# Optimization experiments

Measured on AMD Instinct MI355X. Metric: run time of the kernel, lower is better.

The kernel has to match this reference:

```python
import jax, jax.numpy as jnp
import numpy as np

N_HEADS = 2
WINDOW = 4
BLOCK = 256


def _get_rel_emb(emb, length):
    # emb: [1, 2*WINDOW+1, K] -> [1, 2*length-1, K]
    pad = max(length - (WINDOW + 1), 0)
    start = max((WINDOW + 1) - length, 0)
    e = jnp.pad(emb, ((0, 0), (pad, pad), (0, 0)))
    return e[:, start:start + 2 * length - 1]


def _rel_to_abs(x):
    # x: [b, h, l, 2l-1] -> [b, h, l, l] (skew trick)
    b, h, l, _ = x.shape
    x = jnp.pad(x, ((0, 0), (0, 0), (0, 0), (0, 1))).reshape(b, h, 2 * l * l)
    x = jnp.pad(x, ((0, 0), (0, 0), (0, l - 1))).reshape(b, h, l + 1, 2 * l - 1)
    return x[:, :, :l, l - 1:]


def _abs_to_rel(x):
    # x: [b, h, l, l] -> [b, h, l, 2l-1] (inverse skew)
    b, h, l, _ = x.shape
    x = jnp.pad(x, ((0, 0), (0, 0), (0, 0), (0, l - 1))).reshape(b, h, l * (2 * l - 1))
    x = jnp.pad(x, ((0, 0), (0, 0), (l, 0))).reshape(b, h, l, 2 * l)
    return x[:, :, :, 1:]


def _attention(x, c, attn_mask, Wq, bq, Wk, bk, Wv, bv, Wo, bo, emb_rel_k, emb_rel_v):
    B, C, T = x.shape
    H, K = N_HEADS, C // N_HEADS
    # projections (torch Linear on [B,T,C])
    q = (jnp.einsum('bct,cd->btd', x, Wq) + bq).reshape(B, T, H, K).transpose(0, 2, 1, 3)
    k = (jnp.einsum('bct,cd->btd', c, Wk) + bk).reshape(B, T, H, K).transpose(0, 2, 1, 3)
    v = (jnp.einsum('bct,cd->btd', c, Wv) + bv).reshape(B, T, H, K).transpose(0, 2, 1, 3)
    qs = q / jnp.sqrt(jnp.float32(K))
    scores = jnp.einsum('bhtk,bhsk->bhts', qs, k)  # [B,H,T,T]
    # relative-position key logits (heads_share=True -> single table)
    rel_k = _get_rel_emb(emb_rel_k, T)[0]          # [2T-1, K]
    rel_logits = jnp.einsum('bhtk,rk->bhtr', qs, rel_k)
    scores = scores + _rel_to_abs(rel_logits)
    # proximal bias: -log1p(|i-j|)
    r = jnp.arange(T, dtype=jnp.float32)
    scores = scores - jnp.log1p(jnp.abs(r[:, None] - r[None, :]))[None, None]
    # attn mask + block-local mask (block mask active because mask is given)
    ij = jnp.arange(T)
    block_ok = jnp.abs(ij[:, None] - ij[None, :]) <= BLOCK
    valid = (attn_mask != 0) & block_ok[None, None]
    scores = jnp.where(valid, scores, jnp.float32(-1e4))
    p = jax.nn.softmax(scores, axis=-1)
    out = jnp.einsum('bhts,bhsk->bhtk', p, v)
    # relative-position value contribution
    rel_v = _get_rel_emb(emb_rel_v, T)[0]          # [2T-1, K]
    out = out + jnp.einsum('bhtr,rk->bhtk', _abs_to_rel(p), rel_v)
    out = out.transpose(0, 2, 1, 3).reshape(B, T, C)
    y = jnp.einsum('btd,do->bto', out, Wo) + bo
    return y.transpose(0, 2, 1)  # [B, out_channels, T]


def setup_inputs() -> dict:
    key = jax.random.key(0)
    ks = jax.random.split(key, 8)
    B, C, T = 4, 192, 2048
    K = C // N_HEADS
    s = jnp.float32(0.05)
    rel_std = jnp.float32(K ** -0.5)
    return {
        'x': jax.random.normal(ks[0], (B, C, T), jnp.float32),
        'c': jax.random.normal(ks[1], (B, C, T), jnp.float32),
        'Wq': jax.random.normal(ks[2], (C, C), jnp.float32) * s,
        'bq': jnp.zeros((C,), jnp.float32),
        'Wk': jax.random.normal(ks[3], (C, C), jnp.float32) * s,
        'bk': jnp.zeros((C,), jnp.float32),
        'Wv': jax.random.normal(ks[4], (C, C), jnp.float32) * s,
        'bv': jnp.zeros((C,), jnp.float32),
        'Wo': jax.random.normal(ks[5], (C, C), jnp.float32) * s,
        'bo': jnp.zeros((C,), jnp.float32),
        'emb_rel_k': jax.random.normal(ks[6], (1, 2 * WINDOW + 1, K), jnp.float32) * rel_std,
        'emb_rel_v': jax.random.normal(ks[7], (1, 2 * WINDOW + 1, K), jnp.float32) * rel_std,
        'attn_mask': jnp.ones((B, 1, T, T), jnp.int32),
    }


def reference(x, c, Wq, bq, Wk, bk, Wv, bv, Wo, bo, emb_rel_k, emb_rel_v, attn_mask):
    return _attention(x, c, attn_mask, Wq, bq, Wk, bk, Wv, bv, Wo, bo, emb_rel_k, emb_rel_v)
```

## Files before the change

kernel.cpp:

```cpp
#include <hip/hip_runtime.h>
#include <hip/hip_bf16.h>

#define B_DIM 4
#define C_DIM 192
#define T_SEQ 2048
#define H_DIM 2
#define K_DIM 96
#define BAND 256
#define IT 32
#define NJT 34
#define WSLOT 544
#define WPD 556
#define PRS (2*WPD)
#define XSTR 200
#define PDS 40

typedef __attribute__((ext_vector_type(8))) short bf16x8;
typedef __attribute__((ext_vector_type(4))) short bf16x4;
typedef __attribute__((ext_vector_type(4))) float f32x4;
#define MFMA16 __builtin_amdgcn_mfma_f32_16x16x32_bf16

__device__ __forceinline__ short f2bf_bits(float f) {
    union { __hip_bfloat16 h; short s; } u; u.h = __float2bfloat16(f); return u.s;
}

#define OFF_WT(m)  ((size_t)(m)*73728)
#define OFF_BQS    ((size_t)294912)
#define OFF_RELKBF ((size_t)295680)
#define OFF_RVT    ((size_t)298752)
#define OFF_QBF    ((size_t)304896)
#define OFF_KBF    (OFF_QBF + 3145728)
#define OFF_VTB    (OFF_KBF + 3145728)
#define OFF_OBTC   (OFF_VTB + 3145728)

__global__ __launch_bounds__(256)
void prep_kernel(const float* __restrict__ Wq, const float* __restrict__ Wk,
                 const float* __restrict__ Wv, const float* __restrict__ Wo,
                 const float* __restrict__ bq, const float* __restrict__ relk,
                 const float* __restrict__ relv, char* __restrict__ ws)
{
    const float qscale = 0.14724445972f;
    const int bidx = blockIdx.x;
    const int tid  = threadIdx.x;

    if (bidx < 144) {
        __shared__ float tile[32][33];
        const int mi = bidx / 36, tl = bidx % 36;
        const int R0 = (tl / 6) * 32, C0 = (tl % 6) * 32;
        const float* src = (mi == 0) ? Wq : (mi == 1) ? Wk : (mi == 2) ? Wv : Wo;
        const int r = tid >> 5, cc = tid & 31;
        #pragma unroll
        for (int i = 0; i < 4; ++i) {
            const int rr = r + 8*i;
            tile[rr][cc] = src[(R0 + rr)*C_DIM + C0 + cc];
        }
        __syncthreads();
        short* dst = (short*)(ws + OFF_WT(mi));
        #pragma unroll
        for (int i = 0; i < 4; ++i) {
            const int rr = r + 8*i;
            float v = tile[cc][rr];
            if (mi == 0) v *= qscale;
            dst[(C0 + rr)*C_DIM + R0 + cc] = f2bf_bits(v);
        }
        return;
    }
    if (tid < C_DIM)
        ((float*)(ws + OFF_BQS))[tid] = bq[tid]*qscale;
    short* rkb = (short*)(ws + OFF_RELKBF);
    for (int idx = tid; idx < 16*K_DIM; idx += 256) {
        const int row = idx / K_DIM;
        rkb[idx] = (row < 9) ? f2bf_bits(relk[idx]) : (short)0;
    }
    short* rvt = (short*)(ws + OFF_RVT);
    for (int idx = tid; idx < K_DIM*32; idx += 256) {
        const int col = idx >> 5, dd = idx & 31;
        rvt[idx] = (dd < 9) ? f2bf_bits(relv[dd*K_DIM + col]) : (short)0;
    }
}

__global__ __launch_bounds__(256)
void proj_kernel(const float* __restrict__ x, const float* __restrict__ cin,
                 const float* __restrict__ bk, const float* __restrict__ bv,
                 char* __restrict__ ws)
{
    __shared__ short sb[2*IT*XSTR/2];
    const int hw = blockIdx.x;
    const int L  = (hw & 7)*96 + (hw >> 3);
    const int which = L % 3;
    const int rest  = L / 3;
    const int b  = rest >> 6;
    const int t0 = (rest & 63) * 32;
    const int tid = threadIdx.x;
    const int wave = tid >> 6, lane = tid & 63;
    const int q4 = lane >> 4, lr = lane & 15;

    const float* src = (which == 0) ? x : cin;
    for (int l = tid; l < 1536; l += 256) {
        const int cr = l >> 3, u = l & 7;
        const float4 v4 = *reinterpret_cast<const float4*>(
            src + (size_t)(b*C_DIM + cr)*T_SEQ + t0 + 4*u);
        sb[(4*u+0)*XSTR + cr] = f2bf_bits(v4.x);
        sb[(4*u+1)*XSTR + cr] = f2bf_bits(v4.y);
        sb[(4*u+2)*XSTR + cr] = f2bf_bits(v4.z);
        sb[(4*u+3)*XSTR + cr] = f2bf_bits(v4.w);
    }
    __syncthreads();

    const short* WT = (const short*)(ws + OFF_WT(which));
    f32x4 a[3][2];
    #pragma unroll
    for (int j = 0; j < 3; ++j) {
        a[j][0] = (f32x4){0.f,0.f,0.f,0.f};
        a[j][1] = (f32x4){0.f,0.f,0.f,0.f};
    }
    for (int kc = 0; kc < 6; ++kc) {
        const int ko = kc*32 + q4*8;
        const bf16x8 sf0 = *reinterpret_cast<const bf16x8*>(sb + lr*XSTR + ko);
        const bf16x8 sf1 = *reinterpret_cast<const bf16x8*>(sb + (16 + lr)*XSTR + ko);
        #pragma unroll
        for (int j = 0; j < 3; ++j) {
            const bf16x8 wf = *reinterpret_cast<const bf16x8*>(
                WT + ((3*wave + j)*16 + lr)*C_DIM + ko);
            if (which == 2) {
                a[j][0] = MFMA16(wf, sf0, a[j][0], 0, 0, 0);
                a[j][1] = MFMA16(wf, sf1, a[j][1], 0, 0, 0);
            } else {
                a[j][0] = MFMA16(sf0, wf, a[j][0], 0, 0, 0);
                a[j][1] = MFMA16(sf1, wf, a[j][1], 0, 0, 0);
            }
        }
    }

    const float* bqs = (const float*)(ws + OFF_BQS);
    #pragma unroll
    for (int j = 0; j < 3; ++j) {
        const int dt = 3*wave + j;
        if (which <= 1) {
            const int d = dt*16 + lr, h = d/K_DIM, kk = d%K_DIM;
            const int bh = b*H_DIM + h;
            const float bias = (which == 0) ? bqs[d] : bk[d];
            short* dst = (short*)(ws + (which == 0 ? OFF_QBF : OFF_KBF));
            #pragma unroll
            for (int rt = 0; rt < 2; ++rt)
                #pragma unroll
                for (int e = 0; e < 4; ++e) {
                    const int t = t0 + rt*16 + q4*4 + e;
                    dst[((size_t)bh*T_SEQ + t)*K_DIM + kk] = f2bf_bits(a[j][rt][e] + bias);
                }
        } else {
            short* vtb = (short*)(ws + OFF_VTB);
            #pragma unroll
            for (int rt = 0; rt < 2; ++rt)
                #pragma unroll
                for (int e = 0; e < 4; ++e) {
                    const int d = dt*16 + q4*4 + e, h = d/K_DIM, kk = d%K_DIM;
                    const int bh = b*H_DIM + h;
                    vtb[((size_t)bh*K_DIM + kk)*T_SEQ + t0 + rt*16 + lr] =
                        f2bf_bits(a[j][rt][e] + bv[d]);
                }
        }
    }
}

__global__ __launch_bounds__(1024, 8)
void attn_kernel(const int* __restrict__ mask, char* __restrict__ ws)
{
    __shared__ __align__(16) float ps[IT*WPD];
    __shared__ float lt[257];
    __shared__ __align__(16) char upool[2560];
    float* rl   = (float*)upool;
    short* pd_s = (short*)upool;

    const short* qbf = (const short*)(ws + OFF_QBF);
    const short* kbf = (const short*)(ws + OFF_KBF);
    const short* vtb = (const short*)(ws + OFF_VTB);
    const short* rkb = (const short*)(ws + OFF_RELKBF);
    const short* rvt = (const short*)(ws + OFF_RVT);
    short* obtc = (short*)(ws + OFF_OBTC);

    const int L    = ((blockIdx.x & 7) << 6) + (blockIdx.x >> 3);
    const int b    = L >> 7;
    const int rem  = L & 127;
    const int i0   = (rem >> 1) * IT;
    const int head = rem & 1;
    const int tid  = threadIdx.x;
    const int wave = tid >> 6, lane = tid & 63;
    const int q4 = lane >> 4, lr = lane & 15;
    const int ri = wave & 1, wg = wave >> 1;

    const int jlo  = max(0, i0 - BAND);
    const int jhi  = min(T_SEQ - 1, i0 + IT - 1 + BAND);
    const int wlen = jhi - jlo + 1;
    const size_t qk_base = (size_t)(b*H_DIM + head) * T_SEQ * K_DIM;

    for (int idx = tid; idx < 257; idx += 1024) lt[idx] = log2f((float)(1 + idx));

    bf16x8 qa[3];
    {
        const short* qrow = qbf + qk_base + (size_t)(i0 + ri*16 + lr)*K_DIM + q4*8;
        #pragma unroll
        for (int kc = 0; kc < 3; ++kc)
            qa[kc] = *reinterpret_cast<const bf16x8*>(qrow + kc*32);
    }

    for (int jt = wg; jt < NJT; jt += 8) {
        int jr = jlo + jt*16 + lr;
        if (jr > T_SEQ-1) jr = T_SEQ-1;
        const short* krow = kbf + qk_base + (size_t)jr*K_DIM + q4*8;
        f32x4 s = {0.f,0.f,0.f,0.f};
        #pragma unroll
        for (int kc = 0; kc < 3; ++kc)
            s = MFMA16(qa[kc], *reinterpret_cast<const bf16x8*>(krow + kc*32), s, 0, 0, 0);
        float* pr = ps + (ri*16 + q4*4)*WPD + jt*16 + lr;
        pr[0*WPD] = s[0]; pr[1*WPD] = s[1]; pr[2*WPD] = s[2]; pr[3*WPD] = s[3];
    }
    if (wg == 7) {
        const short* krow = rkb + lr*K_DIM + q4*8;
        f32x4 rs = {0.f,0.f,0.f,0.f};
        #pragma unroll
        for (int kc = 0; kc < 3; ++kc)
            rs = MFMA16(qa[kc], *reinterpret_cast<const bf16x8*>(krow + kc*32), rs, 0, 0, 0);
        if (lr < 9) {
            #pragma unroll
            for (int e = 0; e < 4; ++e)
                rl[(ri*16 + q4*4 + e)*9 + lr] = rs[e];
        }
    }
    __syncthreads();

    {
        const int r = tid >> 5, sj = tid & 31;
        const int i = i0 + r;
        const int* mrow = mask + ((size_t)b*T_SEQ + i)*T_SEQ;
        float* prow = ps + r*WPD;
        float vals[20];
        float m = -INFINITY;
        #pragma unroll
        for (int mm = 0; mm < 5; ++mm) {
            const int j0 = 4*sj + 128*mm;
            float4 pv = make_float4(0.f,0.f,0.f,0.f);
            int4 mv = make_int4(0,0,0,0);
            if (j0 < wlen) {
                pv = *reinterpret_cast<const float4*>(prow + j0);
                mv = *reinterpret_cast<const int4*>(mrow + jlo + j0);
            }
            const float pe[4] = {pv.x, pv.y, pv.z, pv.w};
            const int me[4] = {mv.x, mv.y, mv.z, mv.w};
            #pragma unroll
            for (int e = 0; e < 4; ++e) {
                const int j = j0 + e;
                float val = -INFINITY;
                if (j0 < wlen && j < wlen) {
                    const int dd = jlo + j - i;
                    const int ad = dd < 0 ? -dd : dd;
                    if (ad <= BAND && me[e] != 0) {
                        val = pe[e] - lt[ad];
                        if ((unsigned)(dd + 4) <= 8u) val += rl[r*9 + dd + 4];
                    }
                }
                vals[mm*4 + e] = val;
                m = fmaxf(m, val);
            }
        }
        #pragma unroll
        for (int off = 16; off > 0; off >>= 1) m = fmaxf(m, __shfl_xor(m, off, 64));
        if (m == -INFINITY) m = 0.f;
        float ssum = 0.f;
        #pragma unroll
        for (int u = 0; u < 20; ++u) { vals[u] = exp2f(vals[u] - m); ssum += vals[u]; }
        #pragma unroll
        for (int off = 16; off > 0; off >>= 1) ssum += __shfl_xor(ssum, off, 64);
        const float inv = ssum > 0.f ? 1.f/ssum : 0.f;
        short* pbrow = (short*)prow;
        #pragma unroll
        for (int mm = 0; mm < 5; ++mm) {
            const int j0 = 4*sj + 128*mm;
            if (j0 < WSLOT) {
                bf16x4 w;
                #pragma unroll
                for (int e = 0; e < 4; ++e) w[e] = f2bf_bits(vals[mm*4+e]*inv);
                *reinterpret_cast<bf16x4*>(pbrow + j0) = w;
            }
        }
    }
    __syncthreads();

    for (int idx = tid; idx < IT*PDS; idx += 1024) {
        const int r = idx / PDS, kk = idx % PDS;
        short v = 0;
        if (kk < 9) {
            const int jg = i0 + r + kk - 4;
            if (jg >= 0 && jg < T_SEQ)
                v = ((const short*)ps)[r*PRS + (jg - jlo)];
        }
        pd_s[idx] = v;
    }

    f32x4 o = {0.f,0.f,0.f,0.f};
    const int pri = wave & 1, pnt = wave >> 1;
    if (wave < 12) {
        const short* pbh = (const short*)ps;
        const short* vbase = vtb + qk_base + (size_t)(pnt*16 + lr)*T_SEQ;
        for (int kc = 0; kc < NJT/2; ++kc) {
            const bf16x8 pa = *reinterpret_cast<const bf16x8*>(
                pbh + (pri*16 + lr)*PRS + kc*32 + q4*8);
            int tc = jlo + kc*32 + q4*8;
            if (tc > T_SEQ-8) tc = T_SEQ-8;
            const bf16x8 vb = *reinterpret_cast<const bf16x8*>(vbase + tc);
            o = MFMA16(pa, vb, o, 0, 0, 0);
        }
    }
    __syncthreads();

    if (wave < 12) {
        const bf16x8 pda = *reinterpret_cast<const bf16x8*>(pd_s + (pri*16 + lr)*PDS + q4*8);
        const bf16x8 rv  = *reinterpret_cast<const bf16x8*>(rvt + (pnt*16 + lr)*32 + q4*8);
        o = MFMA16(pda, rv, o, 0, 0, 0);
        const int col = head*K_DIM + pnt*16 + lr;
        #pragma unroll
        for (int e = 0; e < 4; ++e) {
            const int i = i0 + pri*16 + q4*4 + e;
            obtc[((size_t)b*T_SEQ + i)*C_DIM + col] = f2bf_bits(o[e]);
        }
    }
}

__global__ __launch_bounds__(256)
void oproj_kernel(const float* __restrict__ bo, float* __restrict__ y,
                  const char* __restrict__ ws)
{
    const int bid = ((blockIdx.x & 7) << 5) + (blockIdx.x >> 3);
    const int b   = bid >> 6;
    const int t0  = (bid & 63) * 32;
    const int tid = threadIdx.x;
    const int wave = tid >> 6, lane = tid & 63;
    const int q4 = lane >> 4, lr = lane & 15;

    const short* WoT  = (const short*)(ws + OFF_WT(3));
    const short* obtc = (const short*)(ws + OFF_OBTC);

    f32x4 a[3][2];
    #pragma unroll
    for (int j = 0; j < 3; ++j) {
        a[j][0] = (f32x4){0.f,0.f,0.f,0.f};
        a[j][1] = (f32x4){0.f,0.f,0.f,0.f};
    }
    for (int kc = 0; kc < 6; ++kc) {
        const int ko = kc*32 + q4*8;
        const bf16x8 bf0 = *reinterpret_cast<const bf16x8*>(
            obtc + ((size_t)b*T_SEQ + t0 + lr)*C_DIM + ko);
        const bf16x8 bf1 = *reinterpret_cast<const bf16x8*>(
            obtc + ((size_t)b*T_SEQ + t0 + 16 + lr)*C_DIM + ko);
        #pragma unroll
        for (int j = 0; j < 3; ++j) {
            const bf16x8 af = *reinterpret_cast<const bf16x8*>(
                WoT + ((3*wave + j)*16 + lr)*C_DIM + ko);
            a[j][0] = MFMA16(af, bf0, a[j][0], 0, 0, 0);
            a[j][1] = MFMA16(af, bf1, a[j][1], 0, 0, 0);
        }
    }
    #pragma unroll
    for (int j = 0; j < 3; ++j) {
        #pragma unroll
        for (int rt = 0; rt < 2; ++rt)
            #pragma unroll
            for (int e = 0; e < 4; ++e) {
                const int d = (3*wave + j)*16 + q4*4 + e;
                y[((size_t)b*C_DIM + d)*T_SEQ + t0 + rt*16 + lr] = a[j][rt][e] + bo[d];
            }
    }
}

extern "C" void kernel_launch(void* const* d_in, const int* in_sizes, int n_in,
                              void* d_out, int out_size, void* d_ws, size_t ws_size,
                              hipStream_t stream)
{
    const float* x    = (const float*)d_in[0];
    const float* c    = (const float*)d_in[1];
    const float* Wq   = (const float*)d_in[2];
    const float* bq   = (const float*)d_in[3];
    const float* Wk   = (const float*)d_in[4];
    const float* bk   = (const float*)d_in[5];
    const float* Wv   = (const float*)d_in[6];
    const float* bv   = (const float*)d_in[7];
    const float* Wo   = (const float*)d_in[8];
    const float* bo   = (const float*)d_in[9];
    const float* relk = (const float*)d_in[10];
    const float* relv = (const float*)d_in[11];
    const int*   mask = (const int*)d_in[12];
    float*       y    = (float*)d_out;
    char*        ws   = (char*)d_ws;

    hipLaunchKernelGGL(prep_kernel, dim3(145), dim3(256), 0, stream,
                       Wq, Wk, Wv, Wo, bq, relk, relv, ws);
    hipLaunchKernelGGL(proj_kernel, dim3(B_DIM*(T_SEQ/32)*3), dim3(256), 0, stream,
                       x, c, bk, bv, ws);
    hipLaunchKernelGGL(attn_kernel, dim3(B_DIM*H_DIM*(T_SEQ/IT)), dim3(1024), 0, stream,
                       mask, ws);
    hipLaunchKernelGGL(oproj_kernel, dim3(B_DIM*(T_SEQ/32)), dim3(256), 0, stream,
                       bo, y, ws);
}
```

Measured before the change: 167.9 us.

## Fuse output projection into attention kernel via last-block atomic counter

Removes the separate oproj kernel launch. Each attention block bumps a per-(batch, row-tile) counter, and whichever of the two head blocks arrives second runs the output projection for that 32-row tile and writes y. The counters are zeroed in prep_kernel. This saves one launch and its tail gap, at the cost of atomics, thread fences, and a serialized epilogue on half the blocks.

```diff
diff --git a/kernel.cpp b/kernel.cpp
--- a/kernel.cpp
+++ b/kernel.cpp
@@ -32,6 +32,7 @@
 #define OFF_KBF    (OFF_QBF + 3145728)
 #define OFF_VTB    (OFF_KBF + 3145728)
 #define OFF_OBTC   (OFF_VTB + 3145728)
+#define OFF_CNT    (OFF_OBTC + 3145728)
 
 __global__ __launch_bounds__(256)
 void prep_kernel(const float* __restrict__ Wq, const float* __restrict__ Wk,
@@ -67,6 +68,10 @@
     }
     if (tid < C_DIM)
         ((float*)(ws + OFF_BQS))[tid] = bq[tid]*qscale;
+    if (tid >= 192 && tid < 192 + 64) {
+        int4* cnt4 = (int4*)(ws + OFF_CNT);
+        cnt4[tid - 192] = make_int4(0, 0, 0, 0);
+    }
     short* rkb = (short*)(ws + OFF_RELKBF);
     for (int idx = tid; idx < 16*K_DIM; idx += 256) {
         const int row = idx / K_DIM;
@@ -164,11 +169,13 @@
 }
 
 __global__ __launch_bounds__(1024, 8)
-void attn_kernel(const int* __restrict__ mask, char* __restrict__ ws)
+void attn_kernel(const int* __restrict__ mask, const float* __restrict__ bo,
+                 float* __restrict__ y, char* __restrict__ ws)
 {
     __shared__ __align__(16) float ps[IT*WPD];
     __shared__ float lt[257];
     __shared__ __align__(16) char upool[2560];
+    __shared__ int tailflag;
     float* rl   = (float*)upool;
     short* pd_s = (short*)upool;
 
@@ -324,51 +331,39 @@
             obtc[((size_t)b*T_SEQ + i)*C_DIM + col] = f2bf_bits(o[e]);
         }
     }
-}
-
-__global__ __launch_bounds__(256)
-void oproj_kernel(const float* __restrict__ bo, float* __restrict__ y,
-                  const char* __restrict__ ws)
-{
-    const int bid = ((blockIdx.x & 7) << 5) + (blockIdx.x >> 3);
-    const int b   = bid >> 6;
-    const int t0  = (bid & 63) * 32;
-    const int tid = threadIdx.x;
-    const int wave = tid >> 6, lane = tid & 63;
-    const int q4 = lane >> 4, lr = lane & 15;
-
-    const short* WoT  = (const short*)(ws + OFF_WT(3));
-    const short* obtc = (const short*)(ws + OFF_OBTC);
-
-    f32x4 a[3][2];
+
+    __threadfence();
+    __syncthreads();
+    if (tid == 0) {
+        int* cnt = (int*)(ws + OFF_CNT);
+        const int old = atomicAdd(cnt + (b*64 + (i0 >> 5)), 1);
+        if (old == 1) __threadfence();
+        tailflag = (old == 1);
+    }
+    __syncthreads();
+    if (!tailflag) return;
+
+    const short* WoT = (const short*)(ws + OFF_WT(3));
     #pragma unroll
-    for (int j = 0; j < 3; ++j) {
-        a[j][0] = (f32x4){0.f,0.f,0.f,0.f};
-        a[j][1] = (f32x4){0.f,0.f,0.f,0.f};
-    }
-    for (int kc = 0; kc < 6; ++kc) {
-        const int ko = kc*32 + q4*8;
-        const bf16x8 bf0 = *reinterpret_cast<const bf16x8*>(
-            obtc + ((size_t)b*T_SEQ + t0 + lr)*C_DIM + ko);
-        const bf16x8 bf1 = *reinterpret_cast<const bf16x8*>(
-            obtc + ((size_t)b*T_SEQ + t0 + 16 + lr)*C_DIM + ko);
-        #pragma unroll
-        for (int j = 0; j < 3; ++j) {
+    for (int u = 0; u < 2; ++u) {
+        const int j = wave + 16*u;
+        if (u == 1 && j >= 24) break;
+        const int dt = j % 12, rt = j / 12;
+        f32x4 a = {0.f,0.f,0.f,0.f};
+        #pragma unroll
+        for (int kc = 0; kc < 6; ++kc) {
+            const int ko = kc*32 + q4*8;
             const bf16x8 af = *reinterpret_cast<const bf16x8*>(
-                WoT + ((3*wave + j)*16 + lr)*C_DIM + ko);
-            a[j][0] = MFMA16(af, bf0, a[j][0], 0, 0, 0);
-            a[j][1] = MFMA16(af, bf1, a[j][1], 0, 0, 0);
-        }
-    }
-    #pragma unroll
-    for (int j = 0; j < 3; ++j) {
-        #pragma unroll
-        for (int rt = 0; rt < 2; ++rt)
-            #pragma unroll
-            for (int e = 0; e < 4; ++e) {
-                const int d = (3*wave + j)*16 + q4*4 + e;
-                y[((size_t)b*C_DIM + d)*T_SEQ + t0 + rt*16 + lr] = a[j][rt][e] + bo[d];
-            }
+                WoT + (size_t)(dt*16 + lr)*C_DIM + ko);
+            const bf16x8 bf = *reinterpret_cast<const bf16x8*>(
+                obtc + ((size_t)b*T_SEQ + i0 + rt*16 + lr)*C_DIM + ko);
+            a = MFMA16(af, bf, a, 0, 0, 0);
+        }
+        #pragma unroll
+        for (int e = 0; e < 4; ++e) {
+            const int d = dt*16 + q4*4 + e;
+            y[((size_t)b*C_DIM + d)*T_SEQ + i0 + rt*16 + lr] = a[e] + bo[d];
+        }
     }
 }
 
@@ -397,7 +392,5 @@
     hipLaunchKernelGGL(proj_kernel, dim3(B_DIM*(T_SEQ/32)*3), dim3(256), 0, stream,
                        x, c, bk, bv, ws);
     hipLaunchKernelGGL(attn_kernel, dim3(B_DIM*H_DIM*(T_SEQ/IT)), dim3(1024), 0, stream,
-                       mask, ws);
-    hipLaunchKernelGGL(oproj_kernel, dim3(B_DIM*(T_SEQ/32)), dim3(256), 0, stream,
-                       bo, y, ws);
-}
+                       mask, bo, y, ws);
+}
```

After: 362.5 us. 116% more time.
